# Kernel optimization log

Hardware: AMD Instinct MI355X
Metric: run time of the kernel (lower is better)

The kernel has to match this reference:

```python
import jax, jax.numpy as jnp
import numpy as np

N, M, DIST, HEADS, D, C, DFFN = 16384, 16, 2, 8, 256, 64, 512
DH = D // HEADS
GRID = 128
BLOCK = 2048  # mirrors torch batch_size loop in find_neighboring_voxels_optimized
EPS = 1e-5


def _neighbors(coords_f, src, m, dist):
    """Blockwise Manhattan-distance topk neighbor gather.
    coords_f: (N,3) float voxel coords; src: (N,D) features.
    Returns (N, m, D) neighbor features, zero-filled where fewer than m in range."""
    n = coords_f.shape[0]
    qblocks = coords_f.reshape(-1, BLOCK, 3)

    def one_block(cb):
        # (BLOCK, N) Manhattan distances
        d = jnp.abs(cb[:, None, :] - coords_f[None, :, :]).sum(-1)
        d = jnp.where(d <= dist, d, jnp.inf)
        vals, idx = jax.lax.top_k(-d, m)          # nearest m (self first: dist 0)
        valid = (vals > -jnp.inf)[..., None]
        return jnp.where(valid, src[idx], jnp.zeros((), src.dtype))

    return jax.lax.map(one_block, qblocks).reshape(n, m, src.shape[-1])


def _layernorm(x, g, b):
    mu = x.mean(-1, keepdims=True)
    var = ((x - mu) ** 2).mean(-1, keepdims=True)
    return (x - mu) * jax.lax.rsqrt(var + EPS) * g + b


def setup_inputs() -> dict:
    key = jax.random.key(0)
    ks = jax.random.split(key, 32)
    p = lambda i, shape, s: jax.random.normal(ks[i], shape, dtype=jnp.float32) * s
    z = lambda shape: jnp.zeros(shape, dtype=jnp.float32)
    o = lambda shape: jnp.ones(shape, dtype=jnp.float32)
    return {
        "coords": jax.random.randint(ks[0], (N, 3), 0, GRID, dtype=jnp.int32),
        "features": jax.random.normal(ks[1], (N, C), dtype=jnp.float32),
        "pe_w1": p(2, (3, D // 2), 0.5), "pe_b1": z((D // 2,)),
        "pe_w2": p(3, (D // 2, D), 0.08), "pe_b2": z((D,)),
        "proj_w": p(4, (C, D), 0.12), "proj_b": z((D,)),
        "wq": p(5, (D, D), 0.06), "bq": z((D,)),
        "wk": p(6, (D, D), 0.06), "bk": z((D,)),
        "wv": p(7, (D, D), 0.06), "bv": z((D,)),
        "wo": p(8, (D, D), 0.06), "bo": z((D,)),
        "ffn_w1": p(9, (D, DFFN), 0.06), "ffn_b1": z((DFFN,)),
        "ffn_w2": p(10, (DFFN, D), 0.04), "ffn_b2": z((D,)),
        "ln_g": o((D,)), "ln_b": z((D,)),
        "fus_w1": p(11, (D, C), 0.06), "fus_b1": z((C,)),
        "fus_w2": p(12, (2 * C, C), 0.09), "fus_b2": z((C,)),
        "bn_g": o((C,)), "bn_b": z((C,)),
    }


def reference(coords, features, pe_w1, pe_b1, pe_w2, pe_b2, proj_w, proj_b,
              wq, bq, wk, bk, wv, bv, wo, bo,
              ffn_w1, ffn_b1, ffn_w2, ffn_b2, ln_g, ln_b,
              fus_w1, fus_b1, fus_w2, fus_b2, bn_g, bn_b):
    coords_f = coords.astype(jnp.float32)
    # dynamic learnable positional encoding on normalized coords
    xn = coords_f / (GRID - 1)
    pe = jax.nn.relu(xn @ pe_w1 + pe_b1) @ pe_w2 + pe_b2
    src = features @ proj_w + proj_b + pe                       # (N, D)

    nf = _neighbors(coords_f, src, M, DIST)                     # (N, M, D)
    query = nf[:, 0, :]                                         # (N, D) self-feature

    # multihead attention: query len 1, key len M, batch N
    q = (query @ wq + bq).reshape(N, HEADS, DH)
    k = (nf @ wk + bk).reshape(N, M, HEADS, DH)
    v = (nf @ wv + bv).reshape(N, M, HEADS, DH)
    scores = jnp.einsum('nhd,nmhd->nhm', q, k) / jnp.sqrt(jnp.float32(DH))
    attn = jax.nn.softmax(scores, axis=-1)
    ao = jnp.einsum('nhm,nmhd->nhd', attn, v).reshape(N, D) @ wo + bo  # (N, D)

    # FFN with residual + LayerNorm (dropout=0 / eval)
    h = jax.nn.relu(ao @ ffn_w1 + ffn_b1) @ ffn_w2 + ffn_b2
    y = _layernorm(ao + h, ln_g, ln_b)                          # (N, D)

    # EnhancedFusion: project, concat, linear, BatchNorm1d (batch stats), ReLU
    t = y @ fus_w1 + fus_b1                                     # (N, C)
    f = jnp.concatenate([features, t], axis=1) @ fus_w2 + fus_b2
    mu = f.mean(0)
    var = ((f - mu) ** 2).mean(0)
    f = (f - mu) * jax.lax.rsqrt(var + EPS) * bn_g + bn_b
    return jax.nn.relu(f)                                       # (N, C)
```

## Files before the change

### kernel.cpp

```cpp
#include <hip/hip_runtime.h>
#include <stdint.h>

typedef unsigned short u16;
typedef unsigned int   u32;
typedef __attribute__((ext_vector_type(8))) short short8;
typedef __attribute__((ext_vector_type(4))) float f32x4;

static constexpr int kN = 16384;
static constexpr float kEPS = 1e-5f;

__device__ __forceinline__ u16 f2bf(float x) {
  u32 u = __float_as_uint(x);
  u32 r = (u + 0x7fffu + ((u >> 16) & 1u)) >> 16;
  return (u16)r;
}
__device__ __forceinline__ void ldbf8(const u16* p, float* o) {
  uint4 v = *(const uint4*)p;
  o[0] = __uint_as_float(v.x << 16);  o[1] = __uint_as_float(v.x & 0xffff0000u);
  o[2] = __uint_as_float(v.y << 16);  o[3] = __uint_as_float(v.y & 0xffff0000u);
  o[4] = __uint_as_float(v.z << 16);  o[5] = __uint_as_float(v.z & 0xffff0000u);
  o[6] = __uint_as_float(v.w << 16);  o[7] = __uint_as_float(v.w & 0xffff0000u);
}


__global__ __launch_bounds__(256) void k_hist(const int* __restrict__ coords,
                                              u32* __restrict__ cnt) {
  int n = blockIdx.x * 256 + threadIdx.x;
  int c = coords[n * 3] * 128 + coords[n * 3 + 1];
  atomicAdd(&cnt[c], 1u);
}

__global__ __launch_bounds__(256) void k_scan(const u32* __restrict__ cnt,
                                              u32* __restrict__ startb) {
  __shared__ u32 tots[256];
  int t = threadIdx.x;
  int base = t * 64;
  u32 s = 0;
  for (int i = 0; i < 64; i++) s += cnt[base + i];
  tots[t] = s;
  __syncthreads();
  if (t == 0) {
    u32 run = 0;
    for (int i = 0; i < 256; i++) { u32 v = tots[i]; tots[i] = run; run += v; }
  }
  __syncthreads();
  u32 run = tots[t];
  for (int i = 0; i < 64; i++) { startb[base + i] = run; run += cnt[base + i]; }
}

__global__ __launch_bounds__(256) void k_scatter(const int* __restrict__ coords,
                                                 const u32* __restrict__ startb,
                                                 u32* __restrict__ cursor,
                                                 u32* __restrict__ pts) {
  int n = blockIdx.x * 256 + threadIdx.x;
  int x = coords[n * 3], y = coords[n * 3 + 1], z = coords[n * 3 + 2];
  int c = x * 128 + y;
  u32 slot = atomicAdd(&cursor[c], 1u);
  pts[startb[c] + slot] = ((u32)z << 14) | (u32)n;
}

__global__ __launch_bounds__(256) void k_select(const int* __restrict__ coords,
                                                const u32* __restrict__ startb,
                                                const u32* __restrict__ cnt,
                                                const u32* __restrict__ pts,
                                                int* __restrict__ idxo) {
  int n = blockIdx.x * 256 + threadIdx.x;
  int x = coords[n * 3], y = coords[n * 3 + 1], z = coords[n * 3 + 2];
  u32 best[16];
#pragma unroll
  for (int j = 0; j < 16; j++) best[j] = 0xFFFFFFFFu;
  const int dxs[13] = {0, -1, 1, 0, 0, -2, 2, 0, 0, -1, -1, 1, 1};
  const int dys[13] = {0, 0, 0, -1, 1, 0, 0, -2, 2, -1, 1, -1, 1};
  const int dbs[13] = {0, 1, 1, 1, 1, 2, 2, 2, 2, 2, 2, 2, 2};
#pragma unroll
  for (int t = 0; t < 13; t++) {
    int xx = x + dxs[t], yy = y + dys[t];
    if (xx < 0 || xx > 127 || yy < 0 || yy > 127) continue;
    int c = xx * 128 + yy;
    u32 s0 = startb[c], e0 = s0 + cnt[c];
    for (u32 i = s0; i < e0; ++i) {
      u32 p = pts[i];
      int zq = (int)(p >> 14);
      int id = (int)(p & 16383u);
      int az = z - zq; az = az < 0 ? -az : az;
      int dd = dbs[t] + az;
      u32 key = (dd <= 2) ? (((u32)dd << 14) | (u32)id) : 0xFFFFFFFFu;
#pragma unroll
      for (int j = 0; j < 16; j++) {
        u32 lo = min(best[j], key);
        u32 hi = max(best[j], key);
        best[j] = lo; key = hi;
      }
    }
  }
#pragma unroll
  for (int j = 0; j < 16; j++)
    idxo[n * 16 + j] = (best[j] == 0xFFFFFFFFu) ? -1 : (int)(best[j] & 16383u);
}

struct WSet {
  const float* s[10]; u16* d[10];
  int K[10]; int N[10]; int dstride[10]; int coff[10];
};

__global__ __launch_bounds__(256) void k_wcast(WSet ws) {
  int w = blockIdx.y;
  const float* S = ws.s[w]; u16* D = ws.d[w];
  int K = ws.K[w], N = ws.N[w], ds = ws.dstride[w], co = ws.coff[w];
  int ntx = N >> 5, tiles = ntx * (K >> 5);
  int t = blockIdx.x;
  if (t >= tiles) return;
  int n0 = (t % ntx) * 32, k0 = (t / ntx) * 32;
  __shared__ float st[32][33];
  int tr = threadIdx.x >> 3, tc4 = (threadIdx.x & 7) * 4;
  float4 v = *(const float4*)(S + (size_t)(k0 + tr) * N + n0 + tc4);
  st[tc4 + 0][tr] = v.x; st[tc4 + 1][tr] = v.y;
  st[tc4 + 2][tr] = v.z; st[tc4 + 3][tr] = v.w;
  __syncthreads();
  u16 o4[4];
  o4[0] = f2bf(st[tr][tc4 + 0]); o4[1] = f2bf(st[tr][tc4 + 1]);
  o4[2] = f2bf(st[tr][tc4 + 2]); o4[3] = f2bf(st[tr][tc4 + 3]);
  *(uint2*)(D + (size_t)(n0 + tr) * ds + co + k0 + tc4) = *(uint2*)o4;
}

__global__ __launch_bounds__(256) void k_bias2(const float* __restrict__ a,
                                               const float* __restrict__ b,
                                               float* __restrict__ o) {
  int t = threadIdx.x;
  o[t] = a[t] + b[t];
}

__global__ __launch_bounds__(256) void k_prep(const int* __restrict__ coords,
                                              const float* __restrict__ feats,
                                              const float* __restrict__ pw1,
                                              const float* __restrict__ pb1,
                                              u16* __restrict__ A1) {
  int r0 = blockIdx.x * 32;
#pragma unroll
  for (int s = 0; s < 3; s++) {
    int j = threadIdx.x + s * 256;
    int row = j / 24, seg = j % 24;
    int n = r0 + row;
    u16 o[8];
    if (seg < 8) {
      const float* fp = feats + (size_t)n * 64 + seg * 8;
      float4 a = *(const float4*)fp;
      float4 b = *(const float4*)(fp + 4);
      o[0] = f2bf(a.x); o[1] = f2bf(a.y); o[2] = f2bf(a.z); o[3] = f2bf(a.w);
      o[4] = f2bf(b.x); o[5] = f2bf(b.y); o[6] = f2bf(b.z); o[7] = f2bf(b.w);
    } else {
      int jj0 = (seg - 8) * 8;
      float x0 = (float)coords[n * 3 + 0] * (1.f / 127.f);
      float x1 = (float)coords[n * 3 + 1] * (1.f / 127.f);
      float x2 = (float)coords[n * 3 + 2] * (1.f / 127.f);
#pragma unroll
      for (int u = 0; u < 8; u++) {
        int jj = jj0 + u;
        float hv = pb1[jj] + x0 * pw1[jj] + x1 * pw1[128 + jj] + x2 * pw1[256 + jj];
        o[u] = f2bf(fmaxf(hv, 0.f));
      }
    }
    *(uint4*)(A1 + (size_t)n * 192 + seg * 8) = *(uint4*)o;
  }
}

template <int ACT, int SF32, int SBF16, int ADD>
__global__ __launch_bounds__(256) void k_mfma_gemm(
    const u16* __restrict__ A, const u16* __restrict__ WT,
    const float* __restrict__ bias,
    float* __restrict__ Cf, u16* __restrict__ Cb,
    const float* __restrict__ Addp,
    int M, int K, int N) {
  __shared__ __align__(16) u16 As[128 * 32];
  __shared__ __align__(16) u16 Bs[128 * 32];
  const int tid = threadIdx.x;
  const int wave = tid >> 6, lane = tid & 63;
  const int bm = blockIdx.y * 128, bn = blockIdx.x * 128;
  const int wr = (wave >> 1) * 64, wc = (wave & 1) * 64;

  f32x4 acc[4][4];
#pragma unroll
  for (int i = 0; i < 4; i++)
#pragma unroll
    for (int j = 0; j < 4; j++)
#pragma unroll
      for (int r = 0; r < 4; r++) acc[i][j][r] = 0.f;

  for (int k0 = 0; k0 < K; k0 += 32) {
#pragma unroll
    for (int i = 0; i < 2; i++) {
      int cb = i * 256 + wave * 64;
      int c = cb + lane;
      int row = c >> 2, ko = (c & 3) * 8;
      int rowb = min(row, N - 1 - bn);
      __builtin_amdgcn_global_load_lds(
          (const __attribute__((address_space(1))) void*)(A + (size_t)(bm + row) * K + k0 + ko),
          (__attribute__((address_space(3))) void*)(As + (size_t)cb * 8), 16, 0, 0);
      __builtin_amdgcn_global_load_lds(
          (const __attribute__((address_space(1))) void*)(WT + (size_t)(bn + rowb) * K + k0 + ko),
          (__attribute__((address_space(3))) void*)(Bs + (size_t)cb * 8), 16, 0, 0);
    }
    __syncthreads();
    short8 af[4], bg[4];
#pragma unroll
    for (int i = 0; i < 4; i++)
      af[i] = *(const short8*)&As[(wr + i * 16 + (lane & 15)) * 32 + (lane >> 4) * 8];
#pragma unroll
    for (int j = 0; j < 4; j++)
      bg[j] = *(const short8*)&Bs[(wc + j * 16 + (lane & 15)) * 32 + (lane >> 4) * 8];
#pragma unroll
    for (int i = 0; i < 4; i++)
#pragma unroll
      for (int j = 0; j < 4; j++)
        acc[i][j] = __builtin_amdgcn_mfma_f32_16x16x32_bf16(af[i], bg[j], acc[i][j], 0, 0, 0);
    __syncthreads();
  }

#pragma unroll
  for (int j = 0; j < 4; j++) {
    int cc = bn + wc + j * 16 + (lane & 15);
    if (cc >= N) continue;
    float bval = bias ? bias[cc] : 0.f;
#pragma unroll
    for (int i = 0; i < 4; i++) {
      int rbase = bm + wr + i * 16 + (lane >> 4) * 4;
#pragma unroll
      for (int r = 0; r < 4; r++) {
        float v = acc[i][j][r] + bval;
        size_t o = (size_t)(rbase + r) * N + cc;
        if (ADD) v += Addp[o];
        if (ACT) v = fmaxf(v, 0.f);
        if (SF32) Cf[o] = v;
        if (SBF16) Cb[o] = f2bf(v);
      }
    }
  }
}

__global__ __launch_bounds__(256) void k_attn(const u16* __restrict__ QKV,
                                              const int* __restrict__ idx,
                                              const float* __restrict__ bq,
                                              const float* __restrict__ bk,
                                              const float* __restrict__ bv,
                                              u16* __restrict__ outp) {
  int gid = blockIdx.x * 256 + threadIdx.x;
  int n = gid >> 3, h = gid & 7;
  const int* ip = idx + n * 16;
  const int hb = h * 32;
  float q[32];
  {
    int i0 = ip[0];
    const u16* qp = QKV + (size_t)i0 * 768 + hb;
#pragma unroll
    for (int j = 0; j < 32; j += 8) ldbf8(qp + j, &q[j]);
#pragma unroll
    for (int j = 0; j < 32; j++) q[j] += bq[hb + j];
  }
  float qbk = 0.f;
#pragma unroll
  for (int j = 0; j < 32; j++) qbk += q[j] * bk[hb + j];
  float s[16]; int ii[16];
#pragma unroll
  for (int m = 0; m < 16; m++) {
    int i = ip[m]; ii[m] = i;
    float d = qbk;
    if (i >= 0) {
      const u16* kp = QKV + (size_t)i * 768 + 256 + hb;
      float kv[32];
#pragma unroll
      for (int j = 0; j < 32; j += 8) ldbf8(kp + j, &kv[j]);
#pragma unroll
      for (int j = 0; j < 32; j++) d += q[j] * kv[j];
    }
    s[m] = d * 0.17677669529663689f;
  }
  float mx = s[0];
#pragma unroll
  for (int m = 1; m < 16; m++) mx = fmaxf(mx, s[m]);
  float sum = 0.f;
#pragma unroll
  for (int m = 0; m < 16; m++) { s[m] = __expf(s[m] - mx); sum += s[m]; }
  float inv = 1.f / sum;
  float o[32];
#pragma unroll
  for (int j = 0; j < 32; j++) o[j] = 0.f;
#pragma unroll
  for (int m = 0; m < 16; m++) {
    if (ii[m] >= 0) {
      const u16* vp = QKV + (size_t)ii[m] * 768 + 512 + hb;
      float vv[32];
#pragma unroll
      for (int j = 0; j < 32; j += 8) ldbf8(vp + j, &vv[j]);
#pragma unroll
      for (int j = 0; j < 32; j++) o[j] += s[m] * vv[j];
    }
  }
  u16* op = outp + (size_t)n * 256 + hb;
#pragma unroll
  for (int j = 0; j < 32; j += 8) {
    u16 tmp[8];
#pragma unroll
    for (int jj = 0; jj < 8; jj++) tmp[jj] = f2bf(o[j + jj] * inv + bv[hb + j + jj]);
    *(uint4*)(op + j) = *(uint4*)tmp;
  }
}

__global__ __launch_bounds__(256) void k_ln(const float* __restrict__ xx,
                                            const float* __restrict__ g,
                                            const float* __restrict__ b,
                                            u16* __restrict__ y) {
  int row = blockIdx.x * 4 + (threadIdx.x >> 6);
  int lane = threadIdx.x & 63;
  float4 a = *(const float4*)(xx + (size_t)row * 256 + lane * 4);
  float x0 = a.x, x1 = a.y, x2 = a.z, x3 = a.w;
  float sm = x0 + x1 + x2 + x3;
#pragma unroll
  for (int off = 1; off < 64; off <<= 1) sm += __shfl_xor(sm, off);
  float mu = sm * (1.f / 256.f);
  float d0 = x0 - mu, d1 = x1 - mu, d2 = x2 - mu, d3 = x3 - mu;
  float sq = d0 * d0 + d1 * d1 + d2 * d2 + d3 * d3;
#pragma unroll
  for (int off = 1; off < 64; off <<= 1) sq += __shfl_xor(sq, off);
  float rstd = rsqrtf(sq * (1.f / 256.f) + kEPS);
  float4 gv = *(const float4*)(g + lane * 4);
  float4 bv4 = *(const float4*)(b + lane * 4);
  u16 o[4];
  o[0] = f2bf(d0 * rstd * gv.x + bv4.x); o[1] = f2bf(d1 * rstd * gv.y + bv4.y);
  o[2] = f2bf(d2 * rstd * gv.z + bv4.z); o[3] = f2bf(d3 * rstd * gv.w + bv4.w);
  *(uint2*)(y + (size_t)row * 256 + lane * 4) = *(uint2*)o;
}

__global__ __launch_bounds__(256) void k_cat(const float* __restrict__ feats,
                                             const u16* __restrict__ t,
                                             u16* __restrict__ cat) {
  int gid = blockIdx.x * 256 + threadIdx.x;
  int e = gid * 8, n = e >> 7, c = e & 127;
  u16 o[8];
  if (c < 64) {
    const float* fp = feats + (size_t)n * 64 + c;
    float4 a = *(const float4*)fp;
    float4 b = *(const float4*)(fp + 4);
    o[0] = f2bf(a.x); o[1] = f2bf(a.y); o[2] = f2bf(a.z); o[3] = f2bf(a.w);
    o[4] = f2bf(b.x); o[5] = f2bf(b.y); o[6] = f2bf(b.z); o[7] = f2bf(b.w);
    *(uint4*)(cat + e) = *(uint4*)o;
  } else {
    *(uint4*)(cat + e) = *(const uint4*)(t + (size_t)n * 64 + (c - 64));
  }
}

__global__ __launch_bounds__(256) void k_stats(const float* __restrict__ f,
                                               float* __restrict__ pS, float* __restrict__ pQ) {
  int col = threadIdx.x & 63, rc = threadIdx.x >> 6;
  int r0 = blockIdx.x * 128 + rc * 32;
  float s = 0.f, q = 0.f;
  for (int r = 0; r < 32; r++) {
    float v = f[(size_t)(r0 + r) * 64 + col];
    s += v; q += v * v;
  }
  __shared__ float ls[4][64], lq[4][64];
  ls[rc][col] = s; lq[rc][col] = q;
  __syncthreads();
  if (rc == 0) {
    s = ls[0][col] + ls[1][col] + ls[2][col] + ls[3][col];
    q = lq[0][col] + lq[1][col] + lq[2][col] + lq[3][col];
    pS[blockIdx.x * 64 + col] = s;
    pQ[blockIdx.x * 64 + col] = q;
  }
}

__global__ __launch_bounds__(64) void k_bnfin(const float* __restrict__ pS,
                                              const float* __restrict__ pQ,
                                              const float* __restrict__ g,
                                              const float* __restrict__ b,
                                              float* __restrict__ coef,
                                              float* __restrict__ shift) {
  int c = threadIdx.x;
  float s = 0.f, q = 0.f;
  for (int i = 0; i < 128; i++) { s += pS[i * 64 + c]; q += pQ[i * 64 + c]; }
  float mu = s * (1.f / 16384.f);
  float var = q * (1.f / 16384.f) - mu * mu;
  float cf = rsqrtf(var + kEPS) * g[c];
  coef[c] = cf;
  shift[c] = b[c] - mu * cf;
}

__global__ __launch_bounds__(256) void k_bnapply(const float* __restrict__ f,
                                                 const float* __restrict__ coef,
                                                 const float* __restrict__ shift,
                                                 float* __restrict__ out) {
  int gid = blockIdx.x * 256 + threadIdx.x;
  int e = gid * 4, col = e & 63;
  float4 v = *(const float4*)(f + e);
  float4 cf = *(const float4*)(coef + col);
  float4 sh = *(const float4*)(shift + col);
  float4 o;
  o.x = fmaxf(v.x * cf.x + sh.x, 0.f);
  o.y = fmaxf(v.y * cf.y + sh.y, 0.f);
  o.z = fmaxf(v.z * cf.z + sh.z, 0.f);
  o.w = fmaxf(v.w * cf.w + sh.w, 0.f);
  *(float4*)(out + e) = o;
}

extern "C" void kernel_launch(void* const* d_in, const int* in_sizes, int n_in,
                              void* d_out, int out_size, void* d_ws, size_t ws_size,
                              hipStream_t stream) {
  (void)in_sizes; (void)n_in; (void)out_size; (void)ws_size;
  const int*   coords = (const int*)d_in[0];
  const float* feats  = (const float*)d_in[1];
  const float* pe_w1  = (const float*)d_in[2];
  const float* pe_b1  = (const float*)d_in[3];
  const float* pe_w2  = (const float*)d_in[4];
  const float* pe_b2  = (const float*)d_in[5];
  const float* proj_w = (const float*)d_in[6];
  const float* proj_b = (const float*)d_in[7];
  const float* wq  = (const float*)d_in[8];
  const float* bq  = (const float*)d_in[9];
  const float* wk  = (const float*)d_in[10];
  const float* bk  = (const float*)d_in[11];
  const float* wv  = (const float*)d_in[12];
  const float* bv  = (const float*)d_in[13];
  const float* wo  = (const float*)d_in[14];
  const float* bo  = (const float*)d_in[15];
  const float* fw1 = (const float*)d_in[16];
  const float* fb1 = (const float*)d_in[17];
  const float* fw2 = (const float*)d_in[18];
  const float* fb2 = (const float*)d_in[19];
  const float* lng = (const float*)d_in[20];
  const float* lnb = (const float*)d_in[21];
  const float* uw1 = (const float*)d_in[22];
  const float* ub1 = (const float*)d_in[23];
  const float* uw2 = (const float*)d_in[24];
  const float* ub2 = (const float*)d_in[25];
  const float* bng = (const float*)d_in[26];
  const float* bnb = (const float*)d_in[27];
  float* out = (float*)d_out;

  char* Wc = (char*)d_ws;
  const size_t MB = 1u << 20;
  u16*   A1    = (u16*)(Wc + 0 * MB);
  u16*   srcb  = (u16*)(Wc + 6 * MB);
  u16*   QKVb  = (u16*)(Wc + 14 * MB);
  u16*   aoInB = (u16*)(Wc + 38 * MB);
  float* aoF   = (float*)(Wc + 46 * MB);
  u16*   aoB   = (u16*)(Wc + 62 * MB);
  u16*   h1B   = (u16*)(Wc + 70 * MB);
  float* xB    = (float*)(Wc + 14 * MB);
  u16*   yB    = (u16*)(Wc + 30 * MB);
  u16*   catB  = (u16*)(Wc + 0 * MB);
  u16*   tBb   = (u16*)(Wc + 4 * MB);
  float* fB    = (float*)(Wc + 6 * MB);

  u16* qkvT  = (u16*)(Wc + 88 * MB);
  u16* woT   = qkvT + 196608;
  u16* fw1T  = woT + 65536;
  u16* fw2T  = fw1T + 131072;
  u16* W1T   = fw2T + 131072;
  u16* uw1T  = W1T + 49152;
  u16* uw2T  = uw1T + 16384;
  float* pbc = (float*)(uw2T + 8192);

  u32* cnt    = (u32*)(Wc + 90 * MB);
  u32* cursor = cnt + 16384;
  u32* startb = cnt + 32768;
  u32* pts    = cnt + 49152;
  int* idxb   = (int*)(cnt + 65536);
  float* pS    = (float*)(cnt + 65536 + 262144);
  float* pQ    = pS + 8192;
  float* coefb = pQ + 8192;
  float* shb   = coefb + 64;

  hipMemsetAsync(cnt, 0, 32768 * sizeof(u32), stream);

  k_hist<<<64, 256, 0, stream>>>(coords, cnt);
  k_scan<<<1, 256, 0, stream>>>(cnt, startb);
  k_scatter<<<64, 256, 0, stream>>>(coords, startb, cursor, pts);
  k_select<<<64, 256, 0, stream>>>(coords, startb, cnt, pts, idxb);

  WSet ws;
  ws.s[0] = wq;     ws.d[0] = qkvT;          ws.K[0] = 256; ws.N[0] = 256; ws.dstride[0] = 256; ws.coff[0] = 0;
  ws.s[1] = wk;     ws.d[1] = qkvT + 65536;  ws.K[1] = 256; ws.N[1] = 256; ws.dstride[1] = 256; ws.coff[1] = 0;
  ws.s[2] = wv;     ws.d[2] = qkvT + 131072; ws.K[2] = 256; ws.N[2] = 256; ws.dstride[2] = 256; ws.coff[2] = 0;
  ws.s[3] = wo;     ws.d[3] = woT;           ws.K[3] = 256; ws.N[3] = 256; ws.dstride[3] = 256; ws.coff[3] = 0;
  ws.s[4] = fw1;    ws.d[4] = fw1T;          ws.K[4] = 256; ws.N[4] = 512; ws.dstride[4] = 256; ws.coff[4] = 0;
  ws.s[5] = fw2;    ws.d[5] = fw2T;          ws.K[5] = 512; ws.N[5] = 256; ws.dstride[5] = 512; ws.coff[5] = 0;
  ws.s[6] = proj_w; ws.d[6] = W1T;           ws.K[6] = 64;  ws.N[6] = 256; ws.dstride[6] = 192; ws.coff[6] = 0;
  ws.s[7] = pe_w2;  ws.d[7] = W1T;           ws.K[7] = 128; ws.N[7] = 256; ws.dstride[7] = 192; ws.coff[7] = 64;
  ws.s[8] = uw1;    ws.d[8] = uw1T;          ws.K[8] = 256; ws.N[8] = 64;  ws.dstride[8] = 256; ws.coff[8] = 0;
  ws.s[9] = uw2;    ws.d[9] = uw2T;          ws.K[9] = 128; ws.N[9] = 64;  ws.dstride[9] = 128; ws.coff[9] = 0;
  k_wcast<<<dim3(128, 10), 256, 0, stream>>>(ws);
  k_bias2<<<1, 256, 0, stream>>>(proj_b, pe_b2, pbc);

  k_prep<<<512, 256, 0, stream>>>(coords, feats, pe_w1, pe_b1, A1);

  k_mfma_gemm<0, 0, 1, 0><<<dim3(2, 128), 256, 0, stream>>>(A1, W1T, pbc, nullptr, srcb, nullptr, kN, 192, 256);
  k_mfma_gemm<0, 0, 1, 0><<<dim3(6, 128), 256, 0, stream>>>(srcb, qkvT, nullptr, nullptr, QKVb, nullptr, kN, 256, 768);

  k_attn<<<512, 256, 0, stream>>>(QKVb, idxb, bq, bk, bv, aoInB);

  k_mfma_gemm<0, 1, 1, 0><<<dim3(2, 128), 256, 0, stream>>>(aoInB, woT, bo, aoF, aoB, nullptr, kN, 256, 256);
  k_mfma_gemm<1, 0, 1, 0><<<dim3(4, 128), 256, 0, stream>>>(aoB, fw1T, fb1, nullptr, h1B, nullptr, kN, 256, 512);
  k_mfma_gemm<0, 1, 0, 1><<<dim3(2, 128), 256, 0, stream>>>(h1B, fw2T, fb2, xB, nullptr, aoF, kN, 512, 256);

  k_ln<<<4096, 256, 0, stream>>>(xB, lng, lnb, yB);

  k_mfma_gemm<0, 0, 1, 0><<<dim3(1, 128), 256, 0, stream>>>(yB, uw1T, ub1, nullptr, tBb, nullptr, kN, 256, 64);
  k_cat<<<1024, 256, 0, stream>>>(feats, tBb, catB);
  k_mfma_gemm<0, 1, 0, 0><<<dim3(1, 128), 256, 0, stream>>>(catB, uw2T, ub2, fB, nullptr, nullptr, kN, 128, 64);

  k_stats<<<128, 256, 0, stream>>>(fB, pS, pQ);
  k_bnfin<<<1, 64, 0, stream>>>(pS, pQ, bng, bnb, coefb, shb);
  k_bnapply<<<1024, 256, 0, stream>>>(fB, coefb, shb, out);
}
```

Before: 276.5 us.

## Fold fusion linears into one GEMM and reorder attention by spatial bucket

The two chained fusion linears (y@fus_w1 then concat@fus_w2) are folded into a single precomputed weight, W2f = [fus_w1·fus_w2_bottom ; fus_w2_top], with a matching bias. The LayerNorm and prep kernels now write straight into a shared 320-wide A2 buffer, which removes one GEMM, the concat kernel and the intermediate buffers. Attention threads also read their row through the spatially sorted point list, so neighboring voxels share cache lines for gathered K/V. The cost is a small per-call weight-fold kernel, and bf16 rounding of the folded product changes numerics slightly.

Result: faster. 268.0 us (-3.1%).

```diff
diff --git a/kernel.cpp b/kernel.cpp
--- a/kernel.cpp
+++ b/kernel.cpp
@@ -99,8 +99,8 @@
 }
 
 struct WSet {
-  const float* s[10]; u16* d[10];
-  int K[10]; int N[10]; int dstride[10]; int coff[10];
+  const float* s[8]; u16* d[8];
+  int K[8]; int N[8]; int dstride[8]; int coff[8];
 };
 
 __global__ __launch_bounds__(256) void k_wcast(WSet ws) {
@@ -130,11 +130,34 @@
   o[t] = a[t] + b[t];
 }
 
+__global__ __launch_bounds__(320) void k_fuse2w(const float* __restrict__ uw1,
+                                                const float* __restrict__ ub1,
+                                                const float* __restrict__ uw2,
+                                                const float* __restrict__ ub2,
+                                                u16* __restrict__ W2f,
+                                                float* __restrict__ bbf) {
+  int n = blockIdx.x;
+  int k = threadIdx.x;
+  if (k < 256) {
+    float s = 0.f;
+    for (int j = 0; j < 64; j++) s += uw1[k * 64 + j] * uw2[(64 + j) * 64 + n];
+    W2f[n * 320 + k] = f2bf(s);
+  } else {
+    W2f[n * 320 + k] = f2bf(uw2[(k - 256) * 64 + n]);
+  }
+  if (k == 0) {
+    float s = ub2[n];
+    for (int j = 0; j < 64; j++) s += ub1[j] * uw2[(64 + j) * 64 + n];
+    bbf[n] = s;
+  }
+}
+
 __global__ __launch_bounds__(256) void k_prep(const int* __restrict__ coords,
                                               const float* __restrict__ feats,
                                               const float* __restrict__ pw1,
                                               const float* __restrict__ pb1,
-                                              u16* __restrict__ A1) {
+                                              u16* __restrict__ A1,
+                                              u16* __restrict__ A2) {
   int r0 = blockIdx.x * 32;
 #pragma unroll
   for (int s = 0; s < 3; s++) {
@@ -148,6 +171,7 @@
       float4 b = *(const float4*)(fp + 4);
       o[0] = f2bf(a.x); o[1] = f2bf(a.y); o[2] = f2bf(a.z); o[3] = f2bf(a.w);
       o[4] = f2bf(b.x); o[5] = f2bf(b.y); o[6] = f2bf(b.z); o[7] = f2bf(b.w);
+      *(uint4*)(A2 + (size_t)n * 320 + 256 + seg * 8) = *(uint4*)o;
     } else {
       int jj0 = (seg - 8) * 8;
       float x0 = (float)coords[n * 3 + 0] * (1.f / 127.f);
@@ -238,13 +262,14 @@
 }
 
 __global__ __launch_bounds__(256) void k_attn(const u16* __restrict__ QKV,
+                                              const u32* __restrict__ pts,
                                               const int* __restrict__ idx,
                                               const float* __restrict__ bq,
                                               const float* __restrict__ bk,
                                               const float* __restrict__ bv,
                                               u16* __restrict__ outp) {
   int gid = blockIdx.x * 256 + threadIdx.x;
-  int n = gid >> 3, h = gid & 7;
+  int n = (int)(pts[gid >> 3] & 16383u), h = gid & 7;
   const int* ip = idx + n * 16;
   const int hb = h * 32;
   float q[32];
@@ -308,7 +333,7 @@
 __global__ __launch_bounds__(256) void k_ln(const float* __restrict__ xx,
                                             const float* __restrict__ g,
                                             const float* __restrict__ b,
-                                            u16* __restrict__ y) {
+                                            u16* __restrict__ A2) {
   int row = blockIdx.x * 4 + (threadIdx.x >> 6);
   int lane = threadIdx.x & 63;
   float4 a = *(const float4*)(xx + (size_t)row * 256 + lane * 4);
@@ -327,25 +352,7 @@
   u16 o[4];
   o[0] = f2bf(d0 * rstd * gv.x + bv4.x); o[1] = f2bf(d1 * rstd * gv.y + bv4.y);
   o[2] = f2bf(d2 * rstd * gv.z + bv4.z); o[3] = f2bf(d3 * rstd * gv.w + bv4.w);
-  *(uint2*)(y + (size_t)row * 256 + lane * 4) = *(uint2*)o;
-}
-
-__global__ __launch_bounds__(256) void k_cat(const float* __restrict__ feats,
-                                             const u16* __restrict__ t,
-                                             u16* __restrict__ cat) {
-  int gid = blockIdx.x * 256 + threadIdx.x;
-  int e = gid * 8, n = e >> 7, c = e & 127;
-  u16 o[8];
-  if (c < 64) {
-    const float* fp = feats + (size_t)n * 64 + c;
-    float4 a = *(const float4*)fp;
-    float4 b = *(const float4*)(fp + 4);
-    o[0] = f2bf(a.x); o[1] = f2bf(a.y); o[2] = f2bf(a.z); o[3] = f2bf(a.w);
-    o[4] = f2bf(b.x); o[5] = f2bf(b.y); o[6] = f2bf(b.z); o[7] = f2bf(b.w);
-    *(uint4*)(cat + e) = *(uint4*)o;
-  } else {
-    *(uint4*)(cat + e) = *(const uint4*)(t + (size_t)n * 64 + (c - 64));
-  }
+  *(uint2*)(A2 + (size_t)row * 320 + lane * 4) = *(uint2*)o;
 }
 
 __global__ __launch_bounds__(256) void k_stats(const float* __restrict__ f,
@@ -444,22 +451,20 @@
   float* aoF   = (float*)(Wc + 46 * MB);
   u16*   aoB   = (u16*)(Wc + 62 * MB);
   u16*   h1B   = (u16*)(Wc + 70 * MB);
+  u16*   A2    = (u16*)(Wc + 86 * MB);
   float* xB    = (float*)(Wc + 14 * MB);
-  u16*   yB    = (u16*)(Wc + 30 * MB);
-  u16*   catB  = (u16*)(Wc + 0 * MB);
-  u16*   tBb   = (u16*)(Wc + 4 * MB);
-  float* fB    = (float*)(Wc + 6 * MB);
-
-  u16* qkvT  = (u16*)(Wc + 88 * MB);
+  float* fB    = (float*)(Wc + 0 * MB);
+
+  u16* qkvT  = (u16*)(Wc + 96 * MB);
   u16* woT   = qkvT + 196608;
   u16* fw1T  = woT + 65536;
   u16* fw2T  = fw1T + 131072;
   u16* W1T   = fw2T + 131072;
-  u16* uw1T  = W1T + 49152;
-  u16* uw2T  = uw1T + 16384;
-  float* pbc = (float*)(uw2T + 8192);
-
-  u32* cnt    = (u32*)(Wc + 90 * MB);
+  u16* W2f   = W1T + 49152;
+  float* pbc = (float*)(W2f + 20480);
+  float* bbf = pbc + 256;
+
+  u32* cnt    = (u32*)(Wc + 98 * MB);
   u32* cursor = cnt + 16384;
   u32* startb = cnt + 32768;
   u32* pts    = cnt + 49152;
@@ -485,27 +490,24 @@
   ws.s[5] = fw2;    ws.d[5] = fw2T;          ws.K[5] = 512; ws.N[5] = 256; ws.dstride[5] = 512; ws.coff[5] = 0;
   ws.s[6] = proj_w; ws.d[6] = W1T;           ws.K[6] = 64;  ws.N[6] = 256; ws.dstride[6] = 192; ws.coff[6] = 0;
   ws.s[7] = pe_w2;  ws.d[7] = W1T;           ws.K[7] = 128; ws.N[7] = 256; ws.dstride[7] = 192; ws.coff[7] = 64;
-  ws.s[8] = uw1;    ws.d[8] = uw1T;          ws.K[8] = 256; ws.N[8] = 64;  ws.dstride[8] = 256; ws.coff[8] = 0;
-  ws.s[9] = uw2;    ws.d[9] = uw2T;          ws.K[9] = 128; ws.N[9] = 64;  ws.dstride[9] = 128; ws.coff[9] = 0;
-  k_wcast<<<dim3(128, 10), 256, 0, stream>>>(ws);
+  k_wcast<<<dim3(128, 8), 256, 0, stream>>>(ws);
   k_bias2<<<1, 256, 0, stream>>>(proj_b, pe_b2, pbc);
-
-  k_prep<<<512, 256, 0, stream>>>(coords, feats, pe_w1, pe_b1, A1);
+  k_fuse2w<<<64, 320, 0, stream>>>(uw1, ub1, uw2, ub2, W2f, bbf);
+
+  k_prep<<<512, 256, 0, stream>>>(coords, feats, pe_w1, pe_b1, A1, A2);
 
   k_mfma_gemm<0, 0, 1, 0><<<dim3(2, 128), 256, 0, stream>>>(A1, W1T, pbc, nullptr, srcb, nullptr, kN, 192, 256);
   k_mfma_gemm<0, 0, 1, 0><<<dim3(6, 128), 256, 0, stream>>>(srcb, qkvT, nullptr, nullptr, QKVb, nullptr, kN, 256, 768);
 
-  k_attn<<<512, 256, 0, stream>>>(QKVb, idxb, bq, bk, bv, aoInB);
+  k_attn<<<512, 256, 0, stream>>>(QKVb, pts, idxb, bq, bk, bv, aoInB);
 
   k_mfma_gemm<0, 1, 1, 0><<<dim3(2, 128), 256, 0, stream>>>(aoInB, woT, bo, aoF, aoB, nullptr, kN, 256, 256);
   k_mfma_gemm<1, 0, 1, 0><<<dim3(4, 128), 256, 0, stream>>>(aoB, fw1T, fb1, nullptr, h1B, nullptr, kN, 256, 512);
   k_mfma_gemm<0, 1, 0, 1><<<dim3(2, 128), 256, 0, stream>>>(h1B, fw2T, fb2, xB, nullptr, aoF, kN, 512, 256);
 
-  k_ln<<<4096, 256, 0, stream>>>(xB, lng, lnb, yB);
-
-  k_mfma_gemm<0, 0, 1, 0><<<dim3(1, 128), 256, 0, stream>>>(yB, uw1T, ub1, nullptr, tBb, nullptr, kN, 256, 64);
-  k_cat<<<1024, 256, 0, stream>>>(feats, tBb, catB);
-  k_mfma_gemm<0, 1, 0, 0><<<dim3(1, 128), 256, 0, stream>>>(catB, uw2T, ub2, fB, nullptr, nullptr, kN, 128, 64);
+  k_ln<<<4096, 256, 0, stream>>>(xB, lng, lnb, A2);
+
+  k_mfma_gemm<0, 1, 0, 0><<<dim3(1, 128), 256, 0, stream>>>(A2, W2f, bbf, fB, nullptr, nullptr, kN, 320, 64);
 
   k_stats<<<128, 256, 0, stream>>>(fB, pS, pQ);
   k_bnfin<<<1, 64, 0, stream>>>(pS, pQ, bng, bnb, coefb, shb);
```
